# Kernel tuning notes

Hardware: AMD Instinct MI355X
Metric: run time of the kernel (lower is better)

The kernel has to match this reference:

```python
import jax, jax.numpy as jnp
import numpy as np

N_NODES = 20000
N_EDGES = 320000  # directed edges, in reverse pairs (2*i, 2*i+1)
F_NODE = 64
F_EDGE = 16
HID = 300
DEPTH = 3
N_GRAPHS = 128


def setup_inputs() -> dict:
    key = jax.random.key(0)
    ks = jax.random.split(key, 16)
    x = jax.random.normal(ks[0], (N_NODES, F_NODE), dtype=jnp.float32)
    edge_attr = jax.random.normal(ks[1], (N_EDGES, F_EDGE), dtype=jnp.float32)
    # build paired directed edges: edge 2*i is (src,dst), edge 2*i+1 is (dst,src)
    half = N_EDGES // 2
    src = jax.random.randint(ks[2], (half,), 0, N_NODES)
    dst = jax.random.randint(ks[3], (half,), 0, N_NODES)
    row = jnp.stack([src, dst], axis=1).reshape(-1)  # [E]
    col = jnp.stack([dst, src], axis=1).reshape(-1)  # [E]
    edge_index = jnp.stack([row, col], axis=0)  # [2, E]
    batch = jnp.sort(jax.random.randint(ks[4], (N_NODES,), 0, N_GRAPHS))
    s = 0.05
    W_init = jax.random.normal(ks[5], (F_NODE + F_EDGE, HID), dtype=jnp.float32) * s
    b_init = jnp.zeros((HID,), dtype=jnp.float32)
    W_convs = jax.random.normal(ks[6], (DEPTH, HID, HID), dtype=jnp.float32) * s
    b_convs = jnp.zeros((DEPTH, HID), dtype=jnp.float32)
    W_e2n = jax.random.normal(ks[7], (F_NODE + HID, HID), dtype=jnp.float32) * s
    b_e2n = jnp.zeros((HID,), dtype=jnp.float32)
    W_ffn = jax.random.normal(ks[8], (HID, 1), dtype=jnp.float32) * s
    b_ffn = jnp.zeros((1,), dtype=jnp.float32)
    return {"x": x, "edge_attr": edge_attr, "edge_index": edge_index, "batch": batch,
            "W_init": W_init, "b_init": b_init, "W_convs": W_convs, "b_convs": b_convs,
            "W_e2n": W_e2n, "b_e2n": b_e2n, "W_ffn": W_ffn, "b_ffn": b_ffn}


def _rev(h):
    # swap each consecutive forward/reverse edge pair
    e = h.shape[0]
    return h.reshape(e // 2, 2, -1)[:, ::-1, :].reshape(e, -1)


def reference(x, edge_attr, edge_index, batch, W_init, b_init, W_convs, b_convs,
              W_e2n, b_e2n, W_ffn, b_ffn):
    row, col = edge_index[0], edge_index[1]
    # h_0 = act(edge_init(cat([x[row], edge_attr])))
    h0 = jax.nn.relu(jnp.concatenate([x[row], edge_attr], axis=1) @ W_init + b_init)
    h = h0
    for l in range(DEPTH):
        # DMPNNConv: scatter-add edge features to target nodes, gather at source,
        # subtract reverse-edge message, apply Linear
        a = jax.ops.segment_sum(h, col, num_segments=N_NODES)  # [N, H]
        h = (a[row] - _rev(h)) @ W_convs[l] + b_convs[l]
        h = jax.nn.relu(h + h0)  # skip then activation; dropout is eval no-op
    # final conv's a_message only
    s = jax.ops.segment_sum(h, col, num_segments=N_NODES)  # [N, H]
    q = jnp.concatenate([x, s], axis=1)
    hn = jax.nn.relu(q @ W_e2n + b_e2n)  # [N, H]
    pooled = jax.ops.segment_sum(hn, batch, num_segments=N_GRAPHS)  # [G, H]
    return (pooled @ W_ffn + b_ffn).squeeze(-1)  # [G]
```

## Files before the change

kernel.cpp:

```cpp
#include <hip/hip_runtime.h>
#include <hip/hip_bf16.h>

typedef unsigned short ushort_t;
typedef __attribute__((ext_vector_type(8))) short short8;
typedef __attribute__((ext_vector_type(4))) float f32x4;

#define N_NODES 20000
#define N_EDGES 320000
#define F_NODE 64
#define F_EDGE 16
#define HID 300
#define HP 320
#define NTILES 20
#define DEPTH 3
#define N_GRAPHS 128
#define KE2N 384
#define ATS 328

#define WFRAG_USHORT_PER_LAYER (10 * NTILES * 64 * 8)
#define W2FRAG_USHORT (NTILES * 64 * 8)
#define WE2NFRAG_USHORT (12 * NTILES * 64 * 8)

__device__ __forceinline__ float bf2f(ushort_t u) {
    union { unsigned int i; float f; } v;
    v.i = ((unsigned int)u) << 16;
    return v.f;
}

__device__ __forceinline__ unsigned int fpack(float lo, float hi) {
#if __has_builtin(__builtin_amdgcn_cvt_pk_bf16_f32)
    auto r = __builtin_amdgcn_cvt_pk_bf16_f32(lo, hi);
    union { decltype(r) b; unsigned int u; } v;
    v.b = r;
    return v.u;
#else
    union { float f; unsigned int i; } a, b;
    a.f = lo; b.f = hi;
    return ((a.i + 0x8000u) >> 16) | ((b.i + 0x8000u) & 0xffff0000u);
#endif
}
__device__ __forceinline__ ushort_t f2bf(float f) {
    return (ushort_t)(fpack(f, 0.f) & 0xffffu);
}

__global__ __launch_bounds__(256) void csr_hist(
    const int* __restrict__ col, int* __restrict__ deg)
{
    int e = blockIdx.x * 256 + threadIdx.x;
    atomicAdd(&deg[col[e]], 1);
}

__global__ __launch_bounds__(256) void csr_scan(
    const int* __restrict__ deg, int* __restrict__ offsets,
    int* __restrict__ cursor)
{
    __shared__ int sums[256];
    const int t = threadIdx.x;
    const int CH = 79;
    int base = t * CH;
    int local = 0;
    for (int i = 0; i < CH; ++i) {
        int idx = base + i;
        if (idx < N_NODES) local += deg[idx];
    }
    sums[t] = local;
    __syncthreads();
    for (int off = 1; off < 256; off <<= 1) {
        int v = (t >= off) ? sums[t - off] : 0;
        __syncthreads();
        sums[t] += v;
        __syncthreads();
    }
    int run = (t > 0) ? sums[t - 1] : 0;
    for (int i = 0; i < CH; ++i) {
        int idx = base + i;
        if (idx < N_NODES) {
            offsets[idx] = run;
            cursor[idx] = run;
            run += deg[idx];
        }
    }
}

__global__ __launch_bounds__(256) void csr_fill(
    const int* __restrict__ col, int* __restrict__ cursor,
    int* __restrict__ eid)
{
    int e = blockIdx.x * 256 + threadIdx.x;
    int pos = atomicAdd(&cursor[col[e]], 1);
    eid[pos] = e;
}

__global__ __launch_bounds__(256) void ghist(
    const int* __restrict__ batch, int* __restrict__ gdeg)
{
    int n = blockIdx.x * 256 + threadIdx.x;
    if (n < N_NODES) atomicAdd(&gdeg[batch[n]], 1);
}

__global__ __launch_bounds__(128) void gscan(
    const int* __restrict__ gdeg, int* __restrict__ goff)
{
    __shared__ int s[128];
    int t = threadIdx.x;
    int d = gdeg[t];
    s[t] = d;
    __syncthreads();
    for (int off = 1; off < 128; off <<= 1) {
        int v = (t >= off) ? s[t - off] : 0;
        __syncthreads();
        s[t] += v;
        __syncthreads();
    }
    goff[t] = s[t] - d;
    if (t == 127) goff[128] = s[127];
}

__global__ __launch_bounds__(64) void wfrag_build(
    const float* __restrict__ W_convs, ushort_t* __restrict__ wfrag)
{
    const int c = blockIdx.x, t = blockIdx.y, l = blockIdx.z;
    const int lane = threadIdx.x;
    const int k0 = c * 32 + (lane >> 4) * 8;
    const int n  = t * 16 + (lane & 15);
    ushort_t* dst = wfrag + (size_t)l * WFRAG_USHORT_PER_LAYER
                  + ((size_t)(c * NTILES + t) * 64 + lane) * 8;
    const float* Wl = W_convs + (size_t)l * HID * HID;
    #pragma unroll
    for (int j = 0; j < 8; ++j) {
        int k = k0 + j;
        float v = (k < HID && n < HID) ? Wl[(long)k * HID + n] : 0.f;
        dst[j] = f2bf(v);
    }
}

__global__ __launch_bounds__(64) void wfrag2_build(
    const float* __restrict__ W_e2n, ushort_t* __restrict__ wfrag2)
{
    const int c = blockIdx.x, t = blockIdx.y;
    const int lane = threadIdx.x;
    const int k0 = c * 32 + (lane >> 4) * 8;
    const int n  = t * 16 + (lane & 15);
    ushort_t* dst = wfrag2 + ((size_t)(c * NTILES + t) * 64 + lane) * 8;
    #pragma unroll
    for (int j = 0; j < 8; ++j) {
        int k = k0 + j;
        float v = (k < F_NODE + HID && n < HID) ? W_e2n[(long)k * HID + n] : 0.f;
        dst[j] = f2bf(v);
    }
}

__global__ __launch_bounds__(64) void w2frag_build(
    const float* __restrict__ W2, ushort_t* __restrict__ w2frag)
{
    const int t = blockIdx.x;
    const int lane = threadIdx.x;
    const int k0 = (lane >> 4) * 8;
    const int n  = t * 16 + (lane & 15);
    ushort_t* dst = w2frag + ((size_t)t * 64 + lane) * 8;
    #pragma unroll
    for (int j = 0; j < 8; ++j) {
        int k = k0 + j;
        float v = (k < F_EDGE && n < HID) ? W2[(long)k * HID + n] : 0.f;
        dst[j] = f2bf(v);
    }
}


__global__ __launch_bounds__(256) void node_init_gemm(
    const float* __restrict__ x, const float* __restrict__ W_init,
    const float* __restrict__ b_init, ushort_t* __restrict__ xW1b)
{
    __shared__ float xs[16 * 64];
    const int tid = threadIdx.x;
    const long n0 = (long)blockIdx.x * 16;
    for (int i = tid; i < 16 * 64; i += 256) xs[i] = x[n0 * 64 + i];
    __syncthreads();
    const int nl = tid >> 4, ct = tid & 15;
    for (int q = 0; q < 19; ++q) {
        int c = ct + 16 * q;
        if (c < HID) {
            float acc = b_init[c];
            #pragma unroll 8
            for (int k = 0; k < 64; ++k)
                acc = fmaf(xs[nl * 64 + k], W_init[(long)k * HID + c], acc);
            xW1b[(n0 + nl) * HID + c] = f2bf(acc);
        }
    }
}

template<bool UPDATE>
__global__ __launch_bounds__(256) void fused_conv(
    ushort_t* h, const ushort_t* __restrict__ Sb,
    const ushort_t* __restrict__ xW1b, const float* __restrict__ edge_attr,
    const int* __restrict__ row, const ushort_t* __restrict__ w2frag,
    const ushort_t* __restrict__ wfrag_l)
{
    __shared__ ushort_t At[32 * ATS];
    __shared__ int rows[32];
    const int tid = threadIdx.x;
    const int wave = tid >> 6, lane = tid & 63;
    const int quad = lane >> 4, m = lane & 15;
    const long e0 = (long)blockIdx.x * 32;
    if (tid < 32) rows[tid] = row[e0 + tid];

    {
        short8 a_ea[2];
        #pragma unroll
        for (int mt = 0; mt < 2; ++mt) {
            union { uint4 u4; short8 s8; } af;
            if (quad < 2) {
                const float* eap = edge_attr + (e0 + mt * 16 + m) * 16 + quad * 8;
                float4 v0 = *(const float4*)eap;
                float4 v1 = *(const float4*)(eap + 4);
                af.u4.x = fpack(v0.x, v0.y); af.u4.y = fpack(v0.z, v0.w);
                af.u4.z = fpack(v1.x, v1.y); af.u4.w = fpack(v1.z, v1.w);
            } else {
                af.u4.x = 0; af.u4.y = 0; af.u4.z = 0; af.u4.w = 0;
            }
            a_ea[mt] = af.s8;
        }
        const int nt0 = wave * 5;
        #pragma unroll
        for (int t = 0; t < 5; ++t) {
            short8 b = *(const short8*)(w2frag + ((size_t)(nt0 + t) * 64 + lane) * 8);
            #pragma unroll
            for (int mt = 0; mt < 2; ++mt) {
                f32x4 pc = (f32x4){0.f, 0.f, 0.f, 0.f};
                pc = __builtin_amdgcn_mfma_f32_16x16x32_bf16(a_ea[mt], b, pc, 0, 0, 0);
                int c = (nt0 + t) * 16 + m;
                #pragma unroll
                for (int r = 0; r < 4; ++r)
                    At[(mt * 16 + quad * 4 + r) * ATS + c] = f2bf(pc[r]);
            }
        }
    }
    __syncthreads();

    for (int i = tid; i < 16 * 80; i += 256) {
        int p = i / 80, g = i % 80;
        int c0 = 4 * g;
        int la = 2 * p, lb = 2 * p + 1;
        uint2 oa, ob;
        if (g < 75) {
            long Ea = e0 + la, Eb = e0 + lb;
            int ra = rows[la], rb = rows[lb];
            ushort4 xa = *(const ushort4*)&xW1b[(long)ra * HID + c0];
            ushort4 xb = *(const ushort4*)&xW1b[(long)rb * HID + c0];
            ushort4 pa = *(const ushort4*)&At[la * ATS + c0];
            ushort4 pb = *(const ushort4*)&At[lb * ATS + c0];
            float h0a[4], h0b[4];
            h0a[0] = fmaxf(bf2f(xa.x) + bf2f(pa.x), 0.f);
            h0a[1] = fmaxf(bf2f(xa.y) + bf2f(pa.y), 0.f);
            h0a[2] = fmaxf(bf2f(xa.z) + bf2f(pa.z), 0.f);
            h0a[3] = fmaxf(bf2f(xa.w) + bf2f(pa.w), 0.f);
            h0b[0] = fmaxf(bf2f(xb.x) + bf2f(pb.x), 0.f);
            h0b[1] = fmaxf(bf2f(xb.y) + bf2f(pb.y), 0.f);
            h0b[2] = fmaxf(bf2f(xb.z) + bf2f(pb.z), 0.f);
            h0b[3] = fmaxf(bf2f(xb.w) + bf2f(pb.w), 0.f);
            if (UPDATE) {
                ushort4 wa = *(const ushort4*)&h[Ea * HP + c0];
                ushort4 wb = *(const ushort4*)&h[Eb * HP + c0];
                ushort4 sa = *(const ushort4*)&Sb[(long)ra * HID + c0];
                ushort4 sb = *(const ushort4*)&Sb[(long)rb * HID + c0];
                oa.x = fpack(fmaxf(bf2f(sa.x) - bf2f(wb.x) + h0a[0], 0.f),
                             fmaxf(bf2f(sa.y) - bf2f(wb.y) + h0a[1], 0.f));
                oa.y = fpack(fmaxf(bf2f(sa.z) - bf2f(wb.z) + h0a[2], 0.f),
                             fmaxf(bf2f(sa.w) - bf2f(wb.w) + h0a[3], 0.f));
                ob.x = fpack(fmaxf(bf2f(sb.x) - bf2f(wa.x) + h0b[0], 0.f),
                             fmaxf(bf2f(sb.y) - bf2f(wa.y) + h0b[1], 0.f));
                ob.y = fpack(fmaxf(bf2f(sb.z) - bf2f(wa.z) + h0b[2], 0.f),
                             fmaxf(bf2f(sb.w) - bf2f(wa.w) + h0b[3], 0.f));
            } else {
                oa.x = fpack(h0a[0], h0a[1]); oa.y = fpack(h0a[2], h0a[3]);
                ob.x = fpack(h0b[0], h0b[1]); ob.y = fpack(h0b[2], h0b[3]);
            }
        } else {
            oa.x = 0; oa.y = 0;
            ob = oa;
        }
        *(uint2*)&At[la * ATS + c0] = oa;
        *(uint2*)&At[lb * ATS + c0] = ob;
    }
    __syncthreads();

    const int nt0 = wave * 5;
    f32x4 acc[5][2];
    #pragma unroll
    for (int t = 0; t < 5; ++t)
        #pragma unroll
        for (int mt = 0; mt < 2; ++mt)
            acc[t][mt] = (f32x4){0.f, 0.f, 0.f, 0.f};

    for (int c = 0; c < 10; ++c) {
        short8 a[2];
        #pragma unroll
        for (int mt = 0; mt < 2; ++mt)
            a[mt] = *(const short8*)&At[(mt * 16 + m) * ATS + c * 32 + quad * 8];
        #pragma unroll
        for (int t = 0; t < 5; ++t) {
            short8 b = *(const short8*)(wfrag_l
                + ((size_t)(c * NTILES + nt0 + t) * 64 + lane) * 8);
            #pragma unroll
            for (int mt = 0; mt < 2; ++mt)
                acc[t][mt] = __builtin_amdgcn_mfma_f32_16x16x32_bf16(
                    a[mt], b, acc[t][mt], 0, 0, 0);
        }
    }
    #pragma unroll
    for (int t = 0; t < 5; ++t) {
        int col = (nt0 + t) * 16 + m;
        if (col >= HID) continue;
        #pragma unroll
        for (int mt = 0; mt < 2; ++mt) {
            long rbase = (e0 + mt * 16 + quad * 4) * HP + col;
            #pragma unroll
            for (int r = 0; r < 4; ++r)
                h[rbase + (long)r * HP] = f2bf(acc[t][mt][r]);
        }
    }
}

__global__ __launch_bounds__(256) void edge_update_mfma(
    ushort_t* h, const ushort_t* __restrict__ Sb,
    const ushort_t* __restrict__ xW1b, const float* __restrict__ edge_attr,
    const int* __restrict__ row, const ushort_t* __restrict__ w2frag)
{
    __shared__ ushort_t Pt[32 * ATS];
    __shared__ int rows[32];
    const int tid = threadIdx.x;
    const int wave = tid >> 6, lane = tid & 63;
    const int quad = lane >> 4, m = lane & 15;
    const long e0 = (long)blockIdx.x * 32;
    if (tid < 32) rows[tid] = row[e0 + tid];

    {
        short8 a_ea[2];
        #pragma unroll
        for (int mt = 0; mt < 2; ++mt) {
            union { uint4 u4; short8 s8; } af;
            if (quad < 2) {
                const float* eap = edge_attr + (e0 + mt * 16 + m) * 16 + quad * 8;
                float4 v0 = *(const float4*)eap;
                float4 v1 = *(const float4*)(eap + 4);
                af.u4.x = fpack(v0.x, v0.y); af.u4.y = fpack(v0.z, v0.w);
                af.u4.z = fpack(v1.x, v1.y); af.u4.w = fpack(v1.z, v1.w);
            } else {
                af.u4.x = 0; af.u4.y = 0; af.u4.z = 0; af.u4.w = 0;
            }
            a_ea[mt] = af.s8;
        }
        const int nt0 = wave * 5;
        #pragma unroll
        for (int t = 0; t < 5; ++t) {
            short8 b = *(const short8*)(w2frag + ((size_t)(nt0 + t) * 64 + lane) * 8);
            #pragma unroll
            for (int mt = 0; mt < 2; ++mt) {
                f32x4 pc = (f32x4){0.f, 0.f, 0.f, 0.f};
                pc = __builtin_amdgcn_mfma_f32_16x16x32_bf16(a_ea[mt], b, pc, 0, 0, 0);
                int c = (nt0 + t) * 16 + m;
                #pragma unroll
                for (int r = 0; r < 4; ++r)
                    Pt[(mt * 16 + quad * 4 + r) * ATS + c] = f2bf(pc[r]);
            }
        }
    }
    __syncthreads();

    for (int i = tid; i < 16 * 75; i += 256) {
        int p = i / 75, g = i % 75;
        int c0 = 4 * g;
        int la = 2 * p, lb = 2 * p + 1;
        long Ea = e0 + la, Eb = e0 + lb;
        int ra = rows[la], rb = rows[lb];
        ushort4 wa = *(const ushort4*)&h[Ea * HP + c0];
        ushort4 wb = *(const ushort4*)&h[Eb * HP + c0];
        ushort4 sa = *(const ushort4*)&Sb[(long)ra * HID + c0];
        ushort4 sb = *(const ushort4*)&Sb[(long)rb * HID + c0];
        ushort4 xa = *(const ushort4*)&xW1b[(long)ra * HID + c0];
        ushort4 xb = *(const ushort4*)&xW1b[(long)rb * HID + c0];
        ushort4 pa = *(const ushort4*)&Pt[la * ATS + c0];
        ushort4 pb = *(const ushort4*)&Pt[lb * ATS + c0];
        float h0a[4], h0b[4];
        h0a[0] = fmaxf(bf2f(xa.x) + bf2f(pa.x), 0.f);
        h0a[1] = fmaxf(bf2f(xa.y) + bf2f(pa.y), 0.f);
        h0a[2] = fmaxf(bf2f(xa.z) + bf2f(pa.z), 0.f);
        h0a[3] = fmaxf(bf2f(xa.w) + bf2f(pa.w), 0.f);
        h0b[0] = fmaxf(bf2f(xb.x) + bf2f(pb.x), 0.f);
        h0b[1] = fmaxf(bf2f(xb.y) + bf2f(pb.y), 0.f);
        h0b[2] = fmaxf(bf2f(xb.z) + bf2f(pb.z), 0.f);
        h0b[3] = fmaxf(bf2f(xb.w) + bf2f(pb.w), 0.f);
        uint2 oa, ob;
        oa.x = fpack(fmaxf(bf2f(sa.x) - bf2f(wb.x) + h0a[0], 0.f),
                     fmaxf(bf2f(sa.y) - bf2f(wb.y) + h0a[1], 0.f));
        oa.y = fpack(fmaxf(bf2f(sa.z) - bf2f(wb.z) + h0a[2], 0.f),
                     fmaxf(bf2f(sa.w) - bf2f(wb.w) + h0a[3], 0.f));
        ob.x = fpack(fmaxf(bf2f(sb.x) - bf2f(wa.x) + h0b[0], 0.f),
                     fmaxf(bf2f(sb.y) - bf2f(wa.y) + h0b[1], 0.f));
        ob.y = fpack(fmaxf(bf2f(sb.z) - bf2f(wa.z) + h0b[2], 0.f),
                     fmaxf(bf2f(sb.w) - bf2f(wa.w) + h0b[3], 0.f));
        *(uint2*)&h[Ea * HP + c0] = oa;
        *(uint2*)&h[Eb * HP + c0] = ob;
    }
}

__global__ __launch_bounds__(256) void gather_sum(
    const ushort_t* __restrict__ src, const int* __restrict__ offsets,
    const int* __restrict__ ends, const int* __restrict__ eid,
    const float* __restrict__ bias, ushort_t* __restrict__ Sb)
{
    long idx = (long)blockIdx.x * 256 + threadIdx.x;
    if (idx >= (long)N_NODES * 75) return;
    int n = (int)(idx / 75);
    int g = (int)(idx % 75);
    int beg = offsets[n], end = ends[n];
    float a0 = 0.f, a1 = 0.f, a2 = 0.f, a3 = 0.f;
    float b0 = 0.f, b1 = 0.f, b2 = 0.f, b3 = 0.f;
    int j = beg;
    for (; j + 1 < end; j += 2) {
        int e0i = eid[j], e1i = eid[j + 1];
        ushort4 v0 = ((const ushort4*)src)[(long)e0i * (HP / 4) + g];
        ushort4 v1 = ((const ushort4*)src)[(long)e1i * (HP / 4) + g];
        a0 += bf2f(v0.x); a1 += bf2f(v0.y); a2 += bf2f(v0.z); a3 += bf2f(v0.w);
        b0 += bf2f(v1.x); b1 += bf2f(v1.y); b2 += bf2f(v1.z); b3 += bf2f(v1.w);
    }
    if (j < end) {
        int e0i = eid[j];
        ushort4 v0 = ((const ushort4*)src)[(long)e0i * (HP / 4) + g];
        a0 += bf2f(v0.x); a1 += bf2f(v0.y); a2 += bf2f(v0.z); a3 += bf2f(v0.w);
    }
    float4 bv = *(const float4*)&bias[4 * g];
    uint2 o;
    o.x = fpack(a0 + b0 + bv.x, a1 + b1 + bv.y);
    o.y = fpack(a2 + b2 + bv.z, a3 + b3 + bv.w);
    *(uint2*)&Sb[(long)n * HID + 4 * g] = o;
}

__global__ __launch_bounds__(256) void gather_ab(
    const ushort_t* __restrict__ src, const int* __restrict__ offsets,
    const int* __restrict__ ends, const int* __restrict__ eid,
    ushort_t* __restrict__ Ab)
{
    long idx = (long)blockIdx.x * 256 + threadIdx.x;
    if (idx >= (long)N_NODES * 75) return;
    int n = (int)(idx / 75);
    int g = (int)(idx % 75);
    int beg = offsets[n], end = ends[n];
    float a0 = 0.f, a1 = 0.f, a2 = 0.f, a3 = 0.f;
    float b0 = 0.f, b1 = 0.f, b2 = 0.f, b3 = 0.f;
    int j = beg;
    for (; j + 1 < end; j += 2) {
        int e0i = eid[j], e1i = eid[j + 1];
        ushort4 v0 = ((const ushort4*)src)[(long)e0i * (HP / 4) + g];
        ushort4 v1 = ((const ushort4*)src)[(long)e1i * (HP / 4) + g];
        a0 += bf2f(v0.x); a1 += bf2f(v0.y); a2 += bf2f(v0.z); a3 += bf2f(v0.w);
        b0 += bf2f(v1.x); b1 += bf2f(v1.y); b2 += bf2f(v1.z); b3 += bf2f(v1.w);
    }
    if (j < end) {
        int e0i = eid[j];
        ushort4 v0 = ((const ushort4*)src)[(long)e0i * (HP / 4) + g];
        a0 += bf2f(v0.x); a1 += bf2f(v0.y); a2 += bf2f(v0.z); a3 += bf2f(v0.w);
    }
    uint2 o;
    o.x = fpack(a0 + b0, a1 + b1);
    o.y = fpack(a2 + b2, a3 + b3);
    *(uint2*)&Ab[(long)n * KE2N + 64 + 4 * g] = o;
}

__global__ __launch_bounds__(256) void x_fill(
    const float* __restrict__ x, ushort_t* __restrict__ Ab)
{
    long idx = (long)blockIdx.x * 256 + threadIdx.x;
    if (idx >= (long)N_NODES * 21) return;
    int n = (int)(idx / 21);
    int q = (int)(idx % 21);
    if (q < 16) {
        float4 v = *(const float4*)&x[(long)n * 64 + 4 * q];
        uint2 o;
        o.x = fpack(v.x, v.y);
        o.y = fpack(v.z, v.w);
        *(uint2*)&Ab[(long)n * KE2N + 4 * q] = o;
    } else {
        uint2 o; o.x = 0; o.y = 0;
        *(uint2*)&Ab[(long)n * KE2N + 364 + 4 * (q - 16)] = o;
    }
}

__global__ __launch_bounds__(256) void e2n_mfma(
    const ushort_t* __restrict__ Ab, const ushort_t* __restrict__ wfrag2,
    const float* __restrict__ b_e2n, float* __restrict__ hn)
{
    const int tid = threadIdx.x;
    const int wave = tid >> 6, lane = tid & 63;
    const int quad = lane >> 4, m = lane & 15;
    const long n0 = (long)blockIdx.x * 64;
    const int nt0 = wave * 5;

    f32x4 acc[5][4];
    #pragma unroll
    for (int t = 0; t < 5; ++t)
        #pragma unroll
        for (int mt = 0; mt < 4; ++mt)
            acc[t][mt] = (f32x4){0.f, 0.f, 0.f, 0.f};

    for (int c = 0; c < 12; ++c) {
        short8 a[4];
        #pragma unroll
        for (int mt = 0; mt < 4; ++mt) {
            long r = n0 + mt * 16 + m;
            if (r > N_NODES - 1) r = N_NODES - 1;
            a[mt] = *(const short8*)(Ab + r * KE2N + c * 32 + quad * 8);
        }
        #pragma unroll
        for (int t = 0; t < 5; ++t) {
            short8 b = *(const short8*)(wfrag2
                + ((size_t)(c * NTILES + nt0 + t) * 64 + lane) * 8);
            #pragma unroll
            for (int mt = 0; mt < 4; ++mt)
                acc[t][mt] = __builtin_amdgcn_mfma_f32_16x16x32_bf16(
                    a[mt], b, acc[t][mt], 0, 0, 0);
        }
    }

    #pragma unroll
    for (int t = 0; t < 5; ++t) {
        int col = (nt0 + t) * 16 + m;
        if (col >= HID) continue;
        float bias = b_e2n[col];
        #pragma unroll
        for (int mt = 0; mt < 4; ++mt) {
            long rw = n0 + mt * 16 + quad * 4;
            #pragma unroll
            for (int r = 0; r < 4; ++r) {
                long rowi = rw + r;
                if (rowi < N_NODES)
                    hn[rowi * HP + col] = fmaxf(acc[t][mt][r] + bias, 0.f);
            }
        }
    }
}

__global__ __launch_bounds__(256) void pool_graph(
    const float* __restrict__ hn, const int* __restrict__ goff,
    float* __restrict__ pooled)
{
    int g = blockIdx.x;
    int beg = goff[g], end = goff[g + 1];
    for (int c = threadIdx.x; c < HID; c += 256) {
        float acc = 0.f;
        for (int n = beg; n < end; ++n)
            acc += hn[(long)n * HP + c];
        pooled[(long)g * HID + c] = acc;
    }
}

__global__ __launch_bounds__(64) void ffn_out(
    const float* __restrict__ pooled, const float* __restrict__ W_ffn,
    const float* __restrict__ b_ffn, float* __restrict__ out)
{
    int g = blockIdx.x;
    int lane = threadIdx.x;
    float s = 0.f;
    for (int c = lane; c < HID; c += 64)
        s += pooled[(long)g * HID + c] * W_ffn[c];
    #pragma unroll
    for (int off = 32; off > 0; off >>= 1)
        s += __shfl_down(s, off, 64);
    if (lane == 0) out[g] = s + b_ffn[0];
}

extern "C" void kernel_launch(void* const* d_in, const int* in_sizes, int n_in,
                              void* d_out, int out_size, void* d_ws, size_t ws_size,
                              hipStream_t stream) {
    const float* x         = (const float*)d_in[0];
    const float* edge_attr = (const float*)d_in[1];
    const int*   edge_index= (const int*)d_in[2];
    const int*   batch     = (const int*)d_in[3];
    const float* W_init    = (const float*)d_in[4];
    const float* b_init    = (const float*)d_in[5];
    const float* W_convs   = (const float*)d_in[6];
    const float* b_convs   = (const float*)d_in[7];
    const float* W_e2n     = (const float*)d_in[8];
    const float* b_e2n     = (const float*)d_in[9];
    const float* W_ffn     = (const float*)d_in[10];
    const float* b_ffn     = (const float*)d_in[11];
    float* out = (float*)d_out;

    const int* row = edge_index;
    const int* col = edge_index + N_EDGES;
    const float* W2 = W_init + (size_t)F_NODE * HID;

    const size_t need = (size_t)N_EDGES * HP * 2
                      + (size_t)N_NODES * HID * 2
                      + (size_t)N_NODES * KE2N * 2
                      + (size_t)N_GRAPHS * HID * 4
                      + (size_t)N_NODES * 4 * 2 + (size_t)N_EDGES * 4
                      + (size_t)DEPTH * WFRAG_USHORT_PER_LAYER * 2
                      + (size_t)WE2NFRAG_USHORT * 2
                      + (size_t)W2FRAG_USHORT * 2
                      + (size_t)(N_GRAPHS + 1 + N_GRAPHS) * 4 + 32768;
    if (ws_size < need) return;

    char* p = (char*)d_ws;
    auto take = [&](size_t bytes) {
        char* q = p;
        p += (bytes + 255) & ~(size_t)255;
        return q;
    };
    ushort_t* h       = (ushort_t*)take((size_t)N_EDGES * HP * 2);
    ushort_t* Sb      = (ushort_t*)take((size_t)N_NODES * HID * 2);
    ushort_t* Ab      = (ushort_t*)take((size_t)N_NODES * KE2N * 2);
    float*    pooled  = (float*)take((size_t)N_GRAPHS * HID * 4);
    int*      cursor  = (int*)take((size_t)N_NODES * 4);
    int*      offsets = (int*)take((size_t)N_NODES * 4);
    int*      eid     = (int*)take((size_t)N_EDGES * 4);
    ushort_t* wfrag   = (ushort_t*)take((size_t)DEPTH * WFRAG_USHORT_PER_LAYER * 2);
    ushort_t* wfrag2  = (ushort_t*)take((size_t)WE2NFRAG_USHORT * 2);
    ushort_t* w2frag  = (ushort_t*)take((size_t)W2FRAG_USHORT * 2);
    int*      gdeg    = (int*)take((size_t)N_GRAPHS * 4);
    int*      goff    = (int*)take((size_t)(N_GRAPHS + 1) * 4);

    ushort_t* xW1b = Ab;
    float*    hn   = (float*)h;

    hipMemsetAsync(cursor, 0, (size_t)N_NODES * 4, stream);
    hipMemsetAsync(gdeg, 0, (size_t)N_GRAPHS * 4, stream);
    csr_hist<<<N_EDGES / 256, 256, 0, stream>>>(col, cursor);
    csr_scan<<<1, 256, 0, stream>>>(cursor, offsets, cursor);
    csr_fill<<<N_EDGES / 256, 256, 0, stream>>>(col, cursor, eid);
    ghist<<<(N_NODES + 255) / 256, 256, 0, stream>>>(batch, gdeg);
    gscan<<<1, 128, 0, stream>>>(gdeg, goff);

    wfrag_build<<<dim3(10, NTILES, DEPTH), 64, 0, stream>>>(W_convs, wfrag);
    wfrag2_build<<<dim3(12, NTILES, 1), 64, 0, stream>>>(W_e2n, wfrag2);
    w2frag_build<<<NTILES, 64, 0, stream>>>(W2, w2frag);

    node_init_gemm<<<N_NODES / 16, 256, 0, stream>>>(x, W_init, b_init, xW1b);

    const int GS_GRID = ((N_NODES * 75) + 255) / 256;

    fused_conv<false><<<N_EDGES / 32, 256, 0, stream>>>(
        h, Sb, xW1b, edge_attr, row, w2frag, wfrag);
    gather_sum<<<GS_GRID, 256, 0, stream>>>(
        h, offsets, cursor, eid, b_convs + 0 * HID, Sb);
    fused_conv<true><<<N_EDGES / 32, 256, 0, stream>>>(
        h, Sb, xW1b, edge_attr, row, w2frag,
        wfrag + 1 * (size_t)WFRAG_USHORT_PER_LAYER);
    gather_sum<<<GS_GRID, 256, 0, stream>>>(
        h, offsets, cursor, eid, b_convs + 1 * HID, Sb);
    fused_conv<true><<<N_EDGES / 32, 256, 0, stream>>>(
        h, Sb, xW1b, edge_attr, row, w2frag,
        wfrag + 2 * (size_t)WFRAG_USHORT_PER_LAYER);
    gather_sum<<<GS_GRID, 256, 0, stream>>>(
        h, offsets, cursor, eid, b_convs + 2 * HID, Sb);
    edge_update_mfma<<<N_EDGES / 32, 256, 0, stream>>>(
        h, Sb, xW1b, edge_attr, row, w2frag);

    x_fill<<<((N_NODES * 21) + 255) / 256, 256, 0, stream>>>(x, Ab);
    gather_ab<<<GS_GRID, 256, 0, stream>>>(h, offsets, cursor, eid, Ab);
    e2n_mfma<<<(N_NODES + 63) / 64, 256, 0, stream>>>(Ab, wfrag2, b_e2n, hn);
    pool_graph<<<N_GRAPHS, 256, 0, stream>>>(hn, goff, pooled);
    ffn_out<<<N_GRAPHS, 64, 0, stream>>>(pooled, W_ffn, b_ffn, out);
}
```

Before: 1.247 ms.

## Shrink edge-state row pitch to 300 and use packed bf16-pair float math

Sets the per-edge hidden-state row pitch from 320 to 300 columns, so the edge-state buffer holds no padding and the gathers and updates move less memory. The elementwise update and gather kernels now unpack bf16 values two at a time into float2 vectors and use packed add and max, aiming to emit packed VALU instructions. The pitch change affects every kernel that reads or writes h. Row starts are no longer 16-byte aligned, which may break any wide loads elsewhere that assumed the 320 pitch.

```diff
diff --git a/kernel.cpp b/kernel.cpp
--- a/kernel.cpp
+++ b/kernel.cpp
@@ -4,13 +4,14 @@
 typedef unsigned short ushort_t;
 typedef __attribute__((ext_vector_type(8))) short short8;
 typedef __attribute__((ext_vector_type(4))) float f32x4;
+typedef __attribute__((ext_vector_type(2))) float f32x2;
 
 #define N_NODES 20000
 #define N_EDGES 320000
 #define F_NODE 64
 #define F_EDGE 16
 #define HID 300
-#define HP 320
+#define HP 300
 #define NTILES 20
 #define DEPTH 3
 #define N_GRAPHS 128
@@ -25,6 +26,22 @@
     union { unsigned int i; float f; } v;
     v.i = ((unsigned int)u) << 16;
     return v.f;
+}
+
+__device__ __forceinline__ f32x2 bfpair(unsigned int u) {
+    union { unsigned int i[2]; f32x2 f; } v;
+    v.i[0] = u << 16;
+    v.i[1] = u & 0xffff0000u;
+    return v.f;
+}
+
+__device__ __forceinline__ f32x2 pmax0(f32x2 a) {
+#if __has_builtin(__builtin_elementwise_max)
+    f32x2 z = {0.f, 0.f};
+    return __builtin_elementwise_max(a, z);
+#else
+    f32x2 r; r.x = fmaxf(a.x, 0.f); r.y = fmaxf(a.y, 0.f); return r;
+#endif
 }
 
 __device__ __forceinline__ unsigned int fpack(float lo, float hi) {
@@ -39,6 +56,7 @@
     return ((a.i + 0x8000u) >> 16) | ((b.i + 0x8000u) & 0xffff0000u);
 #endif
 }
+__device__ __forceinline__ unsigned int fpack2(f32x2 a) { return fpack(a.x, a.y); }
 __device__ __forceinline__ ushort_t f2bf(float f) {
     return (ushort_t)(fpack(f, 0.f) & 0xffffu);
 }
@@ -224,11 +242,11 @@
         #pragma unroll
         for (int t = 0; t < 5; ++t) {
             short8 b = *(const short8*)(w2frag + ((size_t)(nt0 + t) * 64 + lane) * 8);
+            int c = (nt0 + t) * 16 + m;
             #pragma unroll
             for (int mt = 0; mt < 2; ++mt) {
                 f32x4 pc = (f32x4){0.f, 0.f, 0.f, 0.f};
                 pc = __builtin_amdgcn_mfma_f32_16x16x32_bf16(a_ea[mt], b, pc, 0, 0, 0);
-                int c = (nt0 + t) * 16 + m;
                 #pragma unroll
                 for (int r = 0; r < 4; ++r)
                     At[(mt * 16 + quad * 4 + r) * ATS + c] = f2bf(pc[r]);
@@ -245,35 +263,26 @@
         if (g < 75) {
             long Ea = e0 + la, Eb = e0 + lb;
             int ra = rows[la], rb = rows[lb];
-            ushort4 xa = *(const ushort4*)&xW1b[(long)ra * HID + c0];
-            ushort4 xb = *(const ushort4*)&xW1b[(long)rb * HID + c0];
-            ushort4 pa = *(const ushort4*)&At[la * ATS + c0];
-            ushort4 pb = *(const ushort4*)&At[lb * ATS + c0];
-            float h0a[4], h0b[4];
-            h0a[0] = fmaxf(bf2f(xa.x) + bf2f(pa.x), 0.f);
-            h0a[1] = fmaxf(bf2f(xa.y) + bf2f(pa.y), 0.f);
-            h0a[2] = fmaxf(bf2f(xa.z) + bf2f(pa.z), 0.f);
-            h0a[3] = fmaxf(bf2f(xa.w) + bf2f(pa.w), 0.f);
-            h0b[0] = fmaxf(bf2f(xb.x) + bf2f(pb.x), 0.f);
-            h0b[1] = fmaxf(bf2f(xb.y) + bf2f(pb.y), 0.f);
-            h0b[2] = fmaxf(bf2f(xb.z) + bf2f(pb.z), 0.f);
-            h0b[3] = fmaxf(bf2f(xb.w) + bf2f(pb.w), 0.f);
+            uint2 xa = *(const uint2*)&xW1b[(long)ra * HID + c0];
+            uint2 xb = *(const uint2*)&xW1b[(long)rb * HID + c0];
+            uint2 pa = *(const uint2*)&At[la * ATS + c0];
+            uint2 pb = *(const uint2*)&At[lb * ATS + c0];
+            f32x2 h0a0 = pmax0(bfpair(xa.x) + bfpair(pa.x));
+            f32x2 h0a1 = pmax0(bfpair(xa.y) + bfpair(pa.y));
+            f32x2 h0b0 = pmax0(bfpair(xb.x) + bfpair(pb.x));
+            f32x2 h0b1 = pmax0(bfpair(xb.y) + bfpair(pb.y));
             if (UPDATE) {
-                ushort4 wa = *(const ushort4*)&h[Ea * HP + c0];
-                ushort4 wb = *(const ushort4*)&h[Eb * HP + c0];
-                ushort4 sa = *(const ushort4*)&Sb[(long)ra * HID + c0];
-                ushort4 sb = *(const ushort4*)&Sb[(long)rb * HID + c0];
-                oa.x = fpack(fmaxf(bf2f(sa.x) - bf2f(wb.x) + h0a[0], 0.f),
-                             fmaxf(bf2f(sa.y) - bf2f(wb.y) + h0a[1], 0.f));
-                oa.y = fpack(fmaxf(bf2f(sa.z) - bf2f(wb.z) + h0a[2], 0.f),
-                             fmaxf(bf2f(sa.w) - bf2f(wb.w) + h0a[3], 0.f));
-                ob.x = fpack(fmaxf(bf2f(sb.x) - bf2f(wa.x) + h0b[0], 0.f),
-                             fmaxf(bf2f(sb.y) - bf2f(wa.y) + h0b[1], 0.f));
-                ob.y = fpack(fmaxf(bf2f(sb.z) - bf2f(wa.z) + h0b[2], 0.f),
-                             fmaxf(bf2f(sb.w) - bf2f(wa.w) + h0b[3], 0.f));
+                uint2 wa = *(const uint2*)&h[Ea * HP + c0];
+                uint2 wb = *(const uint2*)&h[Eb * HP + c0];
+                uint2 sa = *(const uint2*)&Sb[(long)ra * HID + c0];
+                uint2 sb = *(const uint2*)&Sb[(long)rb * HID + c0];
+                oa.x = fpack2(pmax0(bfpair(sa.x) - bfpair(wb.x) + h0a0));
+                oa.y = fpack2(pmax0(bfpair(sa.y) - bfpair(wb.y) + h0a1));
+                ob.x = fpack2(pmax0(bfpair(sb.x) - bfpair(wa.x) + h0b0));
+                ob.y = fpack2(pmax0(bfpair(sb.y) - bfpair(wa.y) + h0b1));
             } else {
-                oa.x = fpack(h0a[0], h0a[1]); oa.y = fpack(h0a[2], h0a[3]);
-                ob.x = fpack(h0b[0], h0b[1]); ob.y = fpack(h0b[2], h0b[3]);
+                oa.x = fpack2(h0a0); oa.y = fpack2(h0a1);
+                ob.x = fpack2(h0b0); ob.y = fpack2(h0b1);
             }
         } else {
             oa.x = 0; oa.y = 0;
@@ -373,32 +382,23 @@
         int la = 2 * p, lb = 2 * p + 1;
         long Ea = e0 + la, Eb = e0 + lb;
         int ra = rows[la], rb = rows[lb];
-        ushort4 wa = *(const ushort4*)&h[Ea * HP + c0];
-        ushort4 wb = *(const ushort4*)&h[Eb * HP + c0];
-        ushort4 sa = *(const ushort4*)&Sb[(long)ra * HID + c0];
-        ushort4 sb = *(const ushort4*)&Sb[(long)rb * HID + c0];
-        ushort4 xa = *(const ushort4*)&xW1b[(long)ra * HID + c0];
-        ushort4 xb = *(const ushort4*)&xW1b[(long)rb * HID + c0];
-        ushort4 pa = *(const ushort4*)&Pt[la * ATS + c0];
-        ushort4 pb = *(const ushort4*)&Pt[lb * ATS + c0];
-        float h0a[4], h0b[4];
-        h0a[0] = fmaxf(bf2f(xa.x) + bf2f(pa.x), 0.f);
-        h0a[1] = fmaxf(bf2f(xa.y) + bf2f(pa.y), 0.f);
-        h0a[2] = fmaxf(bf2f(xa.z) + bf2f(pa.z), 0.f);
-        h0a[3] = fmaxf(bf2f(xa.w) + bf2f(pa.w), 0.f);
-        h0b[0] = fmaxf(bf2f(xb.x) + bf2f(pb.x), 0.f);
-        h0b[1] = fmaxf(bf2f(xb.y) + bf2f(pb.y), 0.f);
-        h0b[2] = fmaxf(bf2f(xb.z) + bf2f(pb.z), 0.f);
-        h0b[3] = fmaxf(bf2f(xb.w) + bf2f(pb.w), 0.f);
+        uint2 wa = *(const uint2*)&h[Ea * HP + c0];
+        uint2 wb = *(const uint2*)&h[Eb * HP + c0];
+        uint2 sa = *(const uint2*)&Sb[(long)ra * HID + c0];
+        uint2 sb = *(const uint2*)&Sb[(long)rb * HID + c0];
+        uint2 xa = *(const uint2*)&xW1b[(long)ra * HID + c0];
+        uint2 xb = *(const uint2*)&xW1b[(long)rb * HID + c0];
+        uint2 pa = *(const uint2*)&Pt[la * ATS + c0];
+        uint2 pb = *(const uint2*)&Pt[lb * ATS + c0];
+        f32x2 h0a0 = pmax0(bfpair(xa.x) + bfpair(pa.x));
+        f32x2 h0a1 = pmax0(bfpair(xa.y) + bfpair(pa.y));
+        f32x2 h0b0 = pmax0(bfpair(xb.x) + bfpair(pb.x));
+        f32x2 h0b1 = pmax0(bfpair(xb.y) + bfpair(pb.y));
         uint2 oa, ob;
-        oa.x = fpack(fmaxf(bf2f(sa.x) - bf2f(wb.x) + h0a[0], 0.f),
-                     fmaxf(bf2f(sa.y) - bf2f(wb.y) + h0a[1], 0.f));
-        oa.y = fpack(fmaxf(bf2f(sa.z) - bf2f(wb.z) + h0a[2], 0.f),
-                     fmaxf(bf2f(sa.w) - bf2f(wb.w) + h0a[3], 0.f));
-        ob.x = fpack(fmaxf(bf2f(sb.x) - bf2f(wa.x) + h0b[0], 0.f),
-                     fmaxf(bf2f(sb.y) - bf2f(wa.y) + h0b[1], 0.f));
-        ob.y = fpack(fmaxf(bf2f(sb.z) - bf2f(wa.z) + h0b[2], 0.f),
-                     fmaxf(bf2f(sb.w) - bf2f(wa.w) + h0b[3], 0.f));
+        oa.x = fpack2(pmax0(bfpair(sa.x) - bfpair(wb.x) + h0a0));
+        oa.y = fpack2(pmax0(bfpair(sa.y) - bfpair(wb.y) + h0a1));
+        ob.x = fpack2(pmax0(bfpair(sb.x) - bfpair(wa.x) + h0b0));
+        ob.y = fpack2(pmax0(bfpair(sb.y) - bfpair(wa.y) + h0b1));
         *(uint2*)&h[Ea * HP + c0] = oa;
         *(uint2*)&h[Eb * HP + c0] = ob;
     }
@@ -414,25 +414,26 @@
     int n = (int)(idx / 75);
     int g = (int)(idx % 75);
     int beg = offsets[n], end = ends[n];
-    float a0 = 0.f, a1 = 0.f, a2 = 0.f, a3 = 0.f;
-    float b0 = 0.f, b1 = 0.f, b2 = 0.f, b3 = 0.f;
+    f32x2 A0 = {0.f, 0.f}, A1 = {0.f, 0.f};
+    f32x2 B0 = {0.f, 0.f}, B1 = {0.f, 0.f};
     int j = beg;
     for (; j + 1 < end; j += 2) {
         int e0i = eid[j], e1i = eid[j + 1];
-        ushort4 v0 = ((const ushort4*)src)[(long)e0i * (HP / 4) + g];
-        ushort4 v1 = ((const ushort4*)src)[(long)e1i * (HP / 4) + g];
-        a0 += bf2f(v0.x); a1 += bf2f(v0.y); a2 += bf2f(v0.z); a3 += bf2f(v0.w);
-        b0 += bf2f(v1.x); b1 += bf2f(v1.y); b2 += bf2f(v1.z); b3 += bf2f(v1.w);
+        uint2 v0 = ((const uint2*)src)[(long)e0i * (HP / 4) + g];
+        uint2 v1 = ((const uint2*)src)[(long)e1i * (HP / 4) + g];
+        A0 += bfpair(v0.x); A1 += bfpair(v0.y);
+        B0 += bfpair(v1.x); B1 += bfpair(v1.y);
     }
     if (j < end) {
         int e0i = eid[j];
-        ushort4 v0 = ((const ushort4*)src)[(long)e0i * (HP / 4) + g];
-        a0 += bf2f(v0.x); a1 += bf2f(v0.y); a2 += bf2f(v0.z); a3 += bf2f(v0.w);
+        uint2 v0 = ((const uint2*)src)[(long)e0i * (HP / 4) + g];
+        A0 += bfpair(v0.x); A1 += bfpair(v0.y);
     }
     float4 bv = *(const float4*)&bias[4 * g];
+    f32x2 bv0 = {bv.x, bv.y}, bv1 = {bv.z, bv.w};
     uint2 o;
-    o.x = fpack(a0 + b0 + bv.x, a1 + b1 + bv.y);
-    o.y = fpack(a2 + b2 + bv.z, a3 + b3 + bv.w);
+    o.x = fpack2(A0 + B0 + bv0);
+    o.y = fpack2(A1 + B1 + bv1);
     *(uint2*)&Sb[(long)n * HID + 4 * g] = o;
 }
 
@@ -446,24 +447,24 @@
     int n = (int)(idx / 75);
     int g = (int)(idx % 75);
     int beg = offsets[n], end = ends[n];
-    float a0 = 0.f, a1 = 0.f, a2 = 0.f, a3 = 0.f;
-    float b0 = 0.f, b1 = 0.f, b2 = 0.f, b3 = 0.f;
+    f32x2 A0 = {0.f, 0.f}, A1 = {0.f, 0.f};
+    f32x2 B0 = {0.f, 0.f}, B1 = {0.f, 0.f};
     int j = beg;
     for (; j + 1 < end; j += 2) {
         int e0i = eid[j], e1i = eid[j + 1];
-        ushort4 v0 = ((const ushort4*)src)[(long)e0i * (HP / 4) + g];
-        ushort4 v1 = ((const ushort4*)src)[(long)e1i * (HP / 4) + g];
-        a0 += bf2f(v0.x); a1 += bf2f(v0.y); a2 += bf2f(v0.z); a3 += bf2f(v0.w);
-        b0 += bf2f(v1.x); b1 += bf2f(v1.y); b2 += bf2f(v1.z); b3 += bf2f(v1.w);
+        uint2 v0 = ((const uint2*)src)[(long)e0i * (HP / 4) + g];
+        uint2 v1 = ((const uint2*)src)[(long)e1i * (HP / 4) + g];
+        A0 += bfpair(v0.x); A1 += bfpair(v0.y);
+        B0 += bfpair(v1.x); B1 += bfpair(v1.y);
     }
     if (j < end) {
         int e0i = eid[j];
-        ushort4 v0 = ((const ushort4*)src)[(long)e0i * (HP / 4) + g];
-        a0 += bf2f(v0.x); a1 += bf2f(v0.y); a2 += bf2f(v0.z); a3 += bf2f(v0.w);
+        uint2 v0 = ((const uint2*)src)[(long)e0i * (HP / 4) + g];
+        A0 += bfpair(v0.x); A1 += bfpair(v0.y);
     }
     uint2 o;
-    o.x = fpack(a0 + b0, a1 + b1);
-    o.y = fpack(a2 + b2, a3 + b3);
+    o.x = fpack2(A0 + B0);
+    o.y = fpack2(A1 + B1);
     *(uint2*)&Ab[(long)n * KE2N + 64 + 4 * g] = o;
 }
 
```

New measurement: 1.233 ms. No clear change (-1.2%).
